# Performance work log

Measured on AMD Instinct MI355X. Metric: run time of the kernel, lower is better.

Reference implementation:

```python
import jax, jax.numpy as jnp
import numpy as np

N = 100000      # nodes
E = 1600000     # edges
D_IN = 32
D_OUT = 32
K = 2           # propagation hops; module has k+1 alpha scalars


def setup_inputs() -> dict:
    key = jax.random.key(0)
    k1, k2, k3, k4, k5 = jax.random.split(key, 5)
    feat = jax.random.normal(k1, (N, D_IN), dtype=jnp.float32)
    src = jax.random.randint(k2, (E,), 0, N, dtype=jnp.int32)
    dst = jax.random.randint(k3, (E,), 0, N, dtype=jnp.int32)
    stdv = 1.0 / np.sqrt(D_OUT)
    W = jax.random.uniform(k4, (D_OUT, D_IN), dtype=jnp.float32, minval=-stdv, maxval=stdv)
    b = jnp.zeros((D_OUT,), dtype=jnp.float32)
    stdvk = 1.0 / np.sqrt(K)
    alpha = jax.random.uniform(k5, (K + 1,), dtype=jnp.float32, minval=-stdvk, maxval=stdvk)
    return {"feat": feat, "src": src, "dst": dst, "W": W, "b": b, "alpha": alpha}


def reference(feat, src, dst, W, b, alpha):
    n = feat.shape[0]
    # in-degrees (edges point src -> dst; copy_u/sum aggregates at dst)
    deg = jax.ops.segment_sum(jnp.ones_like(dst, dtype=jnp.float32), dst, num_segments=n)
    norm = jnp.maximum(deg, 1.0)[:, None] ** -0.5  # [n,1]

    feats = [feat]
    h = feat
    for _ in range(K):
        h = h * norm                                       # pre-normalize
        h = jax.ops.segment_sum(h[src], dst, num_segments=n)  # SpMM: gather+scatter-add
        h = h * norm                                       # post-normalize
        feats.append(h)

    # result = sum_i fc(alpha_i * feat_i); bias added once per hop term (as in torch)
    result = jnp.zeros((n, W.shape[0]), dtype=jnp.float32)
    for i, f in enumerate(feats):
        result = result + (alpha[i] * f) @ W.T + b
    return result
```

## Files before the change

kernel.cpp:

```cpp
#include <hip/hip_runtime.h>

#define D 32
#define CHUNK 4096
#define BWID 512
#define BSH 9
#define SCAN_T 256
#define SCAN_V 4
#define SCAN_CHUNK 1024

__device__ __forceinline__ unsigned f2bf2(float lo, float hi) {
    union { float f; unsigned u; } a, b;
    a.f = lo; b.f = hi;
    unsigned ra = a.u + 0x7FFFu + ((a.u >> 16) & 1u);
    unsigned rb = b.u + 0x7FFFu + ((b.u >> 16) & 1u);
    return (ra >> 16) | (rb & 0xFFFF0000u);
}
__device__ __forceinline__ void bf2_unpack(unsigned u, float& lo, float& hi) {
    union { unsigned u; float f; } a, b;
    a.u = u << 16; b.u = u & 0xFFFF0000u;
    lo = a.f; hi = b.f;
}


__global__ void p1_count_kernel(const int* __restrict__ dst, int* __restrict__ cnt,
                                int E, int NB) {
    __shared__ int h[256];
    int blk = blockIdx.x, t = threadIdx.x;
    for (int i = t; i < 256; i += 256) h[i] = 0;
    __syncthreads();
    int base = blk * CHUNK;
    int end = min(base + CHUNK, E);
    int tbase = base + t * 16;
    #pragma unroll
    for (int k = 0; k < 4; ++k) {
        int a = tbase + k * 4;
        if (a + 3 < end) {
            int4 d = *(const int4*)(dst + a);
            atomicAdd(&h[d.x >> BSH], 1);
            atomicAdd(&h[d.y >> BSH], 1);
            atomicAdd(&h[d.z >> BSH], 1);
            atomicAdd(&h[d.w >> BSH], 1);
        } else {
            for (int e = a; e < end && e < a + 4; ++e) atomicAdd(&h[dst[e] >> BSH], 1);
        }
    }
    __syncthreads();
    for (int i = t; i < NB; i += 256) cnt[blk * NB + i] = h[i];
}

__global__ void red_kernel(const int* __restrict__ cnt, int* __restrict__ btot,
                           int GB, int NB) {
    __shared__ int s[256];
    int b = blockIdx.x, t = threadIdx.x;
    int acc = 0;
    for (int g = t; g < GB; g += 256) acc += cnt[g * NB + b];
    s[t] = acc;
    __syncthreads();
    for (int off = 128; off > 0; off >>= 1) {
        if (t < off) s[t] += s[t + off];
        __syncthreads();
    }
    if (t == 0) btot[b] = s[0];
}

__global__ void scanb_kernel(const int* __restrict__ btot, int* __restrict__ bbase, int NB) {
    __shared__ int s[256];
    int t = threadIdx.x;
    int v = (t < NB) ? btot[t] : 0;
    s[t] = v;
    __syncthreads();
    for (int off = 1; off < 256; off <<= 1) {
        int x = (t >= off) ? s[t - off] : 0;
        __syncthreads();
        s[t] += x;
        __syncthreads();
    }
    if (t < NB) bbase[t] = s[t] - v;
    if (t == NB - 1) bbase[NB] = s[t];
}

__global__ void off_kernel(const int* __restrict__ cnt, const int* __restrict__ bbase,
                           int* __restrict__ off, int GB, int NB) {
    __shared__ int st[256];
    int b = blockIdx.x, t = threadIdx.x;
    int g0 = 2 * t, g1 = 2 * t + 1;
    int c0 = (g0 < GB) ? cnt[g0 * NB + b] : 0;
    int c1 = (g1 < GB) ? cnt[g1 * NB + b] : 0;
    int pair = c0 + c1;
    st[t] = pair;
    __syncthreads();
    for (int o = 1; o < 256; o <<= 1) {
        int x = (t >= o) ? st[t - o] : 0;
        __syncthreads();
        st[t] += x;
        __syncthreads();
    }
    int ex = bbase[b] + st[t] - pair;
    if (g0 < GB) off[g0 * NB + b] = ex;
    if (g1 < GB) off[g1 * NB + b] = ex + c0;
}

__global__ void p3_scatter_kernel(const int* __restrict__ src, const int* __restrict__ dst,
                                  const int* __restrict__ off, unsigned* __restrict__ ebuf,
                                  int E, int NB) {
    __shared__ int cur[256];
    int blk = blockIdx.x, t = threadIdx.x;
    for (int i = t; i < NB; i += 256) cur[i] = off[blk * NB + i];
    __syncthreads();
    int base = blk * CHUNK;
    int end = min(base + CHUNK, E);
    int tbase = base + t * 16;
    #pragma unroll
    for (int k = 0; k < 4; ++k) {
        int a = tbase + k * 4;
        if (a + 3 < end) {
            int4 d = *(const int4*)(dst + a);
            int4 s = *(const int4*)(src + a);
            int p0 = atomicAdd(&cur[d.x >> BSH], 1);
            int p1 = atomicAdd(&cur[d.y >> BSH], 1);
            int p2 = atomicAdd(&cur[d.z >> BSH], 1);
            int p3 = atomicAdd(&cur[d.w >> BSH], 1);
            ebuf[p0] = ((unsigned)(d.x & (BWID - 1)) << 23) | (unsigned)s.x;
            ebuf[p1] = ((unsigned)(d.y & (BWID - 1)) << 23) | (unsigned)s.y;
            ebuf[p2] = ((unsigned)(d.z & (BWID - 1)) << 23) | (unsigned)s.z;
            ebuf[p3] = ((unsigned)(d.w & (BWID - 1)) << 23) | (unsigned)s.w;
        } else {
            for (int e = a; e < end && e < a + 4; ++e) {
                int dv = dst[e];
                int p = atomicAdd(&cur[dv >> BSH], 1);
                ebuf[p] = ((unsigned)(dv & (BWID - 1)) << 23) | (unsigned)src[e];
            }
        }
    }
}

__global__ void p4_kernel(const unsigned* __restrict__ ebuf, const int* __restrict__ bbase,
                          int* __restrict__ row_start, int* __restrict__ row_end,
                          float* __restrict__ norm, int* __restrict__ csr_src,
                          const float4* __restrict__ feat4, uint4* __restrict__ A1q, int N) {
    __shared__ int deg2[BWID];
    __shared__ int rs[BWID];
    __shared__ int st[256];
    int b = blockIdx.x, t = threadIdx.x;
    int node0 = b << BSH;
    int nn = min(BWID, N - node0);
    int e0 = bbase[b], e1 = bbase[b + 1];
    deg2[t] = 0; deg2[t + 256] = 0;
    __syncthreads();
    for (int j = e0 + t; j < e1; j += 256)
        atomicAdd(&deg2[ebuf[j] >> 23], 1);
    __syncthreads();
    int d0 = deg2[2 * t], d1 = deg2[2 * t + 1];
    int pair = d0 + d1;
    st[t] = pair;
    __syncthreads();
    for (int off = 1; off < 256; off <<= 1) {
        int v = (t >= off) ? st[t - off] : 0;
        __syncthreads();
        st[t] += v;
        __syncthreads();
    }
    int ex = st[t] - pair;
    rs[2 * t] = ex;
    rs[2 * t + 1] = ex + d0;
    __syncthreads();
    #pragma unroll
    for (int k = 0; k < 2; ++k) {
        int i = t + k * 256;
        if (i < nn) {
            int dg = deg2[i];
            int r = e0 + rs[i];
            row_start[node0 + i] = r;
            row_end[node0 + i]   = r + dg;
            norm[node0 + i] = rsqrtf(fmaxf((float)dg, 1.0f));
        }
    }
    __syncthreads();
    for (int j = e0 + t; j < e1; j += 256) {
        unsigned v = ebuf[j];
        int dl = v >> 23;
        int p = atomicAdd(&rs[dl], 1);
        csr_src[e0 + p] = (int)(v & 0x7FFFFF);
    }
    for (int c = t; c < nn * 4; c += 256) {
        int nl = c >> 2, q = c & 3;
        float nv = rsqrtf(fmaxf((float)deg2[nl], 1.0f));
        size_t rf = (size_t)(node0 + nl) * 8 + q * 2;
        float4 f0 = feat4[rf], f1 = feat4[rf + 1];
        uint4 o;
        o.x = f2bf2(f0.x * nv, f0.y * nv);
        o.y = f2bf2(f0.z * nv, f0.w * nv);
        o.z = f2bf2(f1.x * nv, f1.y * nv);
        o.w = f2bf2(f1.z * nv, f1.w * nv);
        A1q[(size_t)(node0 + nl) * 4 + q] = o;
    }
}

__global__ void degpos_kernel(const int* __restrict__ dst, int* __restrict__ deg,
                              int* __restrict__ pos, int E) {
    int t = blockIdx.x * blockDim.x + threadIdx.x;
    int base = t * 4;
    if (base + 3 < E) {
        int4 d = *(const int4*)(dst + base);
        int4 p;
        p.x = atomicAdd(&deg[d.x], 1);
        p.y = atomicAdd(&deg[d.y], 1);
        p.z = atomicAdd(&deg[d.z], 1);
        p.w = atomicAdd(&deg[d.w], 1);
        *(int4*)(pos + base) = p;
    } else if (base < E) {
        for (int e = base; e < E; ++e) pos[e] = atomicAdd(&deg[dst[e]], 1);
    }
}

__global__ void scan1_kernel(const int* __restrict__ deg, int* __restrict__ partial, int n) {
    __shared__ int sdata[SCAN_T];
    int base = blockIdx.x * SCAN_CHUNK + threadIdx.x * SCAN_V;
    int s = 0;
    #pragma unroll
    for (int k = 0; k < SCAN_V; ++k) { int i = base + k; if (i < n) s += deg[i]; }
    sdata[threadIdx.x] = s;
    __syncthreads();
    for (int off = SCAN_T / 2; off > 0; off >>= 1) {
        if (threadIdx.x < off) sdata[threadIdx.x] += sdata[threadIdx.x + off];
        __syncthreads();
    }
    if (threadIdx.x == 0) partial[blockIdx.x] = sdata[0];
}

__global__ void scan2_kernel(int* __restrict__ partial, int nb) {
    __shared__ int sdata[256];
    int v = (threadIdx.x < nb) ? partial[threadIdx.x] : 0;
    sdata[threadIdx.x] = v;
    __syncthreads();
    for (int off = 1; off < 256; off <<= 1) {
        int t = (threadIdx.x >= off) ? sdata[threadIdx.x - off] : 0;
        __syncthreads();
        sdata[threadIdx.x] += t;
        __syncthreads();
    }
    if (threadIdx.x < nb) partial[threadIdx.x] = sdata[threadIdx.x] - v;
}

__global__ void scan3_kernel(const int* __restrict__ deg, const int* __restrict__ partial,
                             int* __restrict__ row_start, int* __restrict__ row_end,
                             float* __restrict__ norm, int n) {
    __shared__ int sdata[SCAN_T];
    int base = blockIdx.x * SCAN_CHUNK + threadIdx.x * SCAN_V;
    int v[SCAN_V];
    int s = 0;
    #pragma unroll
    for (int k = 0; k < SCAN_V; ++k) { int i = base + k; v[k] = (i < n) ? deg[i] : 0; s += v[k]; }
    int self = s;
    sdata[threadIdx.x] = s;
    __syncthreads();
    for (int off = 1; off < SCAN_T; off <<= 1) {
        int t = (threadIdx.x >= off) ? sdata[threadIdx.x - off] : 0;
        __syncthreads();
        sdata[threadIdx.x] += t;
        __syncthreads();
    }
    int run = partial[blockIdx.x] + sdata[threadIdx.x] - self;
    #pragma unroll
    for (int k = 0; k < SCAN_V; ++k) {
        int i = base + k;
        if (i < n) {
            row_start[i] = run;
            row_end[i]   = run + v[k];
            norm[i] = rsqrtf(fmaxf((float)v[k], 1.0f));
            run += v[k];
        }
    }
}

__global__ void fillA_kernel(const int* __restrict__ src, const int* __restrict__ dst,
                             const int* __restrict__ pos, const int* __restrict__ row_start,
                             int* __restrict__ csr_src, int E) {
    int t = blockIdx.x * blockDim.x + threadIdx.x;
    int base = t * 4;
    if (base + 3 < E) {
        int4 d = *(const int4*)(dst + base);
        int4 p = *(const int4*)(pos + base);
        int4 s = *(const int4*)(src + base);
        csr_src[row_start[d.x] + p.x] = s.x;
        csr_src[row_start[d.y] + p.y] = s.y;
        csr_src[row_start[d.z] + p.z] = s.z;
        csr_src[row_start[d.w] + p.w] = s.w;
    } else if (base < E) {
        for (int e = base; e < E; ++e)
            csr_src[row_start[dst[e]] + pos[e]] = src[e];
    }
}

__global__ void prep_kernel(const float4* __restrict__ feat4, const float* __restrict__ norm,
                            uint4* __restrict__ A1q, int nchunk) {
    int i = blockIdx.x * blockDim.x + threadIdx.x;
    if (i >= nchunk) return;
    int v = i >> 2;
    float nv = norm[v];
    float4 f0 = feat4[(size_t)i * 2], f1 = feat4[(size_t)i * 2 + 1];
    uint4 o;
    o.x = f2bf2(f0.x * nv, f0.y * nv);
    o.y = f2bf2(f0.z * nv, f0.w * nv);
    o.z = f2bf2(f1.x * nv, f1.y * nv);
    o.w = f2bf2(f1.z * nv, f1.w * nv);
    A1q[i] = o;
}


#define ACC_EDGE(V)                                              \
    { float lo_, hi_;                                            \
      bf2_unpack((V).x, lo_, hi_); acc[0] += lo_; acc[1] += hi_; \
      bf2_unpack((V).y, lo_, hi_); acc[2] += lo_; acc[3] += hi_; \
      bf2_unpack((V).z, lo_, hi_); acc[4] += lo_; acc[5] += hi_; \
      bf2_unpack((V).w, lo_, hi_); acc[6] += lo_; acc[7] += hi_; }

__global__ __launch_bounds__(256) void gather1_kernel(
        const int* __restrict__ row_start, const int* __restrict__ row_end,
        const int* __restrict__ csr_src, const uint4* __restrict__ A1q,
        const float4* __restrict__ feat4, const float* __restrict__ norm,
        const float* __restrict__ alpha, float4* __restrict__ G,
        uint4* __restrict__ A2q, int n) {
    int wave = blockIdx.x * (blockDim.x >> 6) + (threadIdx.x >> 6);
    int lane = threadIdx.x & 63;
    int g  = lane >> 4;
    int eo = (lane >> 2) & 3;
    int q  = lane & 3;
    int r = wave * 4 + g;
    int s0 = 0, e1 = 0;
    if (r < n) { s0 = row_start[r]; e1 = row_end[r]; }
    float acc[8];
    #pragma unroll
    for (int i = 0; i < 8; ++i) acc[i] = 0.f;
    int j = s0 + eo;
    for (; j + 4 < e1; j += 8) {
        int sa = csr_src[j];
        int sb = csr_src[j + 4];
        uint4 va = A1q[(size_t)sa * 4 + q];
        uint4 vb = A1q[(size_t)sb * 4 + q];
        ACC_EDGE(va);
        ACC_EDGE(vb);
    }
    if (j < e1) {
        int sa = csr_src[j];
        uint4 va = A1q[(size_t)sa * 4 + q];
        ACC_EDGE(va);
    }
    #pragma unroll
    for (int i = 0; i < 8; ++i) {
        acc[i] += __shfl_xor(acc[i], 4);
        acc[i] += __shfl_xor(acc[i], 8);
    }
    if (eo == 0 && r < n) {
        float nv = norm[r];
        float a0 = alpha[0], a1 = alpha[1];
        size_t rf = (size_t)r * 8 + q * 2;
        float4 f0 = feat4[rf], f1 = feat4[rf + 1];
        float h[8];
        #pragma unroll
        for (int i = 0; i < 8; ++i) h[i] = acc[i] * nv;
        G[rf]     = make_float4(fmaf(a1, h[0], a0 * f0.x), fmaf(a1, h[1], a0 * f0.y),
                                fmaf(a1, h[2], a0 * f0.z), fmaf(a1, h[3], a0 * f0.w));
        G[rf + 1] = make_float4(fmaf(a1, h[4], a0 * f1.x), fmaf(a1, h[5], a0 * f1.y),
                                fmaf(a1, h[6], a0 * f1.z), fmaf(a1, h[7], a0 * f1.w));
        uint4 o;
        o.x = f2bf2(h[0] * nv, h[1] * nv);
        o.y = f2bf2(h[2] * nv, h[3] * nv);
        o.z = f2bf2(h[4] * nv, h[5] * nv);
        o.w = f2bf2(h[6] * nv, h[7] * nv);
        A2q[(size_t)r * 4 + q] = o;
    }
}

__global__ __launch_bounds__(256) void gather2_kernel(
        const int* __restrict__ row_start, const int* __restrict__ row_end,
        const int* __restrict__ csr_src, const uint4* __restrict__ A2q,
        const float* __restrict__ norm, const float* __restrict__ alpha,
        const float* __restrict__ W, const float* __restrict__ b,
        float4* __restrict__ G, int n) {
    __shared__ float Wl[D][D + 1];
    __shared__ float pbuf[4][4][D];
    int tid = threadIdx.x;
    for (int k = tid; k < D * D; k += 256) Wl[k >> 5][k & 31] = W[k];
    __syncthreads();

    int wv = tid >> 6;
    int wave = blockIdx.x * 4 + wv;
    int lane = tid & 63;
    int g  = lane >> 4;
    int eo = (lane >> 2) & 3;
    int q  = lane & 3;
    int r = wave * 4 + g;
    int s0 = 0, e1 = 0;
    if (r < n) { s0 = row_start[r]; e1 = row_end[r]; }
    float acc[8];
    #pragma unroll
    for (int i = 0; i < 8; ++i) acc[i] = 0.f;
    int j = s0 + eo;
    for (; j + 4 < e1; j += 8) {
        int sa = csr_src[j];
        int sb = csr_src[j + 4];
        uint4 va = A2q[(size_t)sa * 4 + q];
        uint4 vb = A2q[(size_t)sb * 4 + q];
        ACC_EDGE(va);
        ACC_EDGE(vb);
    }
    if (j < e1) {
        int sa = csr_src[j];
        uint4 va = A2q[(size_t)sa * 4 + q];
        ACC_EDGE(va);
    }
    #pragma unroll
    for (int i = 0; i < 8; ++i) {
        acc[i] += __shfl_xor(acc[i], 4);
        acc[i] += __shfl_xor(acc[i], 8);
    }
    if (eo == 0 && r < n) {
        float nv = norm[r];
        float a2 = alpha[2];
        size_t rf = (size_t)r * 8 + q * 2;
        float4 g0 = G[rf], g1 = G[rf + 1];
        float4 p0 = make_float4(fmaf(a2, acc[0] * nv, g0.x), fmaf(a2, acc[1] * nv, g0.y),
                                fmaf(a2, acc[2] * nv, g0.z), fmaf(a2, acc[3] * nv, g0.w));
        float4 p1 = make_float4(fmaf(a2, acc[4] * nv, g1.x), fmaf(a2, acc[5] * nv, g1.y),
                                fmaf(a2, acc[6] * nv, g1.z), fmaf(a2, acc[7] * nv, g1.w));
        *(float4*)&pbuf[wv][g][q * 8]     = p0;
        *(float4*)&pbuf[wv][g][q * 8 + 4] = p1;
    }
    asm volatile("s_waitcnt lgkmcnt(0)" ::: "memory");

    int o  = lane & 31;
    int rr = lane >> 5;
    #pragma unroll
    for (int rp = 0; rp < 2; ++rp) {
        int gg = rp * 2 + rr;
        int row = wave * 4 + gg;
        if (row < n) {
            float acco = 0.f;
            #pragma unroll
            for (int k = 0; k < D; ++k)
                acco = fmaf(pbuf[wv][gg][k], Wl[o][k], acco);
            ((float*)G)[(size_t)row * D + o] = acco + 3.0f * b[o];
        }
    }
}

extern "C" void kernel_launch(void* const* d_in, const int* in_sizes, int n_in,
                              void* d_out, int out_size, void* d_ws, size_t ws_size,
                              hipStream_t stream) {
    const float* feat  = (const float*)d_in[0];
    const int*   src   = (const int*)  d_in[1];
    const int*   dst   = (const int*)  d_in[2];
    const float* W     = (const float*)d_in[3];
    const float* b     = (const float*)d_in[4];
    const float* alpha = (const float*)d_in[5];

    const int N  = in_sizes[0] / D;
    const int E  = in_sizes[1];
    const int BT = 256;
    const int NB = (N + BWID - 1) >> BSH;
    const int GB = (E + CHUNK - 1) / CHUNK;
    const int gblocks = (N + 15) / 16;
    float4* G = (float4*)d_out;

    size_t needA = ((size_t)32 * N + 2 * (size_t)GB * NB + 2 * NB + 1
                    + 2 * (size_t)E + 3 * (size_t)N) * 4;

    if (ws_size >= needA && NB <= 256 && GB <= 512 && N < (1 << 23)) {
        unsigned* A1q       = (unsigned*)d_ws;
        unsigned* A2q       = A1q + (size_t)16 * N;
        int*      cnt       = (int*)(A2q + (size_t)16 * N);
        int*      off       = cnt + (size_t)GB * NB;
        int*      btot      = off + (size_t)GB * NB;
        int*      bbase     = btot + NB;
        unsigned* ebuf      = (unsigned*)(bbase + NB + 1);
        int*      csr_src   = (int*)(ebuf + E);
        int*      row_start = csr_src + E;
        int*      row_end   = row_start + N;
        float*    norm      = (float*)(row_end + N);

        p1_count_kernel<<<GB, BT, 0, stream>>>(dst, cnt, E, NB);
        red_kernel<<<NB, BT, 0, stream>>>(cnt, btot, GB, NB);
        scanb_kernel<<<1, BT, 0, stream>>>(btot, bbase, NB);
        off_kernel<<<NB, BT, 0, stream>>>(cnt, bbase, off, GB, NB);
        p3_scatter_kernel<<<GB, BT, 0, stream>>>(src, dst, off, ebuf, E, NB);
        p4_kernel<<<NB, BT, 0, stream>>>(ebuf, bbase, row_start, row_end, norm, csr_src,
                                         (const float4*)feat, (uint4*)A1q, N);
        gather1_kernel<<<gblocks, BT, 0, stream>>>(row_start, row_end, csr_src,
                                                   (const uint4*)A1q, (const float4*)feat,
                                                   norm, alpha, G, (uint4*)A2q, N);
        gather2_kernel<<<gblocks, BT, 0, stream>>>(row_start, row_end, csr_src,
                                                   (const uint4*)A2q, norm, alpha,
                                                   W, b, G, N);
    } else {
        const int nb = (N + SCAN_CHUNK - 1) / SCAN_CHUNK;
        const int e4blocks = ((E + 3) / 4 + BT - 1) / BT;
        unsigned* A1q       = (unsigned*)d_ws;
        unsigned* A2q       = A1q + (size_t)16 * N;
        int*      deg       = (int*)(A2q + (size_t)16 * N);
        int*      pos       = deg + N;
        int*      partial   = pos + E;
        int*      row_start = partial + 256;
        int*      row_end   = row_start + N;
        int*      csr_src   = row_end + N;
        float*    norm      = (float*)(csr_src + E);

        hipMemsetAsync(deg, 0, (size_t)N * sizeof(int), stream);
        degpos_kernel<<<e4blocks, BT, 0, stream>>>(dst, deg, pos, E);
        scan1_kernel<<<nb, SCAN_T, 0, stream>>>(deg, partial, N);
        scan2_kernel<<<1, 256, 0, stream>>>(partial, nb);
        scan3_kernel<<<nb, SCAN_T, 0, stream>>>(deg, partial, row_start, row_end, norm, N);
        fillA_kernel<<<e4blocks, BT, 0, stream>>>(src, dst, pos, row_start, csr_src, E);
        prep_kernel<<<(4 * N + BT - 1) / BT, BT, 0, stream>>>(
            (const float4*)feat, norm, (uint4*)A1q, 4 * N);
        gather1_kernel<<<gblocks, BT, 0, stream>>>(row_start, row_end, csr_src,
                                                   (const uint4*)A1q, (const float4*)feat,
                                                   norm, alpha, G, (uint4*)A2q, N);
        gather2_kernel<<<gblocks, BT, 0, stream>>>(row_start, row_end, csr_src,
                                                   (const uint4*)A2q, norm, alpha,
                                                   W, b, G, N);
    }
}
```

Measured before the change: 113.3 us.

## Split feature gathers into two 16-column halves with separate GEMM pass

The bf16 propagated features are stored as two half-width arrays of 16 columns each. Each gather hop runs twice, once per half, so the random-access working set per pass is halved and should fit better in L2/MALL. Each lane now covers 8 edges and 2 quads, and the fused W projection moves out of gather2 into a standalone GEMM kernel. This costs extra launches, reading the CSR index arrays twice per hop, and an extra read/write pass over the output.

```diff
diff --git a/kernel.cpp b/kernel.cpp
--- a/kernel.cpp
+++ b/kernel.cpp
@@ -137,7 +137,8 @@
 __global__ void p4_kernel(const unsigned* __restrict__ ebuf, const int* __restrict__ bbase,
                           int* __restrict__ row_start, int* __restrict__ row_end,
                           float* __restrict__ norm, int* __restrict__ csr_src,
-                          const float4* __restrict__ feat4, uint4* __restrict__ A1q, int N) {
+                          const float* __restrict__ feat,
+                          unsigned* __restrict__ A1h0, unsigned* __restrict__ A1h1, int N) {
     __shared__ int deg2[BWID];
     __shared__ int rs[BWID];
     __shared__ int st[256];
@@ -182,17 +183,14 @@
         int p = atomicAdd(&rs[dl], 1);
         csr_src[e0 + p] = (int)(v & 0x7FFFFF);
     }
-    for (int c = t; c < nn * 4; c += 256) {
-        int nl = c >> 2, q = c & 3;
-        float nv = rsqrtf(fmaxf((float)deg2[nl], 1.0f));
-        size_t rf = (size_t)(node0 + nl) * 8 + q * 2;
-        float4 f0 = feat4[rf], f1 = feat4[rf + 1];
-        uint4 o;
-        o.x = f2bf2(f0.x * nv, f0.y * nv);
-        o.y = f2bf2(f0.z * nv, f0.w * nv);
-        o.z = f2bf2(f1.x * nv, f1.y * nv);
-        o.w = f2bf2(f1.z * nv, f1.w * nv);
-        A1q[(size_t)(node0 + nl) * 4 + q] = o;
+    for (int c = t; c < nn * 16; c += 256) {
+        int i = c >> 4, k = c & 15;
+        float nv = rsqrtf(fmaxf((float)deg2[i], 1.0f));
+        size_t fi = (size_t)(node0 + i) * D + 2 * k;
+        float2 f = *(const float2*)(feat + fi);
+        unsigned u = f2bf2(f.x * nv, f.y * nv);
+        if (k < 8) A1h0[(size_t)(node0 + i) * 8 + k] = u;
+        else       A1h1[(size_t)(node0 + i) * 8 + (k - 8)] = u;
     }
 }
 
@@ -292,23 +290,22 @@
     }
 }
 
-__global__ void prep_kernel(const float4* __restrict__ feat4, const float* __restrict__ norm,
-                            uint4* __restrict__ A1q, int nchunk) {
-    int i = blockIdx.x * blockDim.x + threadIdx.x;
-    if (i >= nchunk) return;
-    int v = i >> 2;
+__global__ void prep_kernel(const float* __restrict__ feat, const float* __restrict__ norm,
+                            unsigned* __restrict__ A1h0, unsigned* __restrict__ A1h1,
+                            int total) {
+    int c = blockIdx.x * blockDim.x + threadIdx.x;
+    if (c >= total) return;
+    int v = c >> 4, k = c & 15;
     float nv = norm[v];
-    float4 f0 = feat4[(size_t)i * 2], f1 = feat4[(size_t)i * 2 + 1];
-    uint4 o;
-    o.x = f2bf2(f0.x * nv, f0.y * nv);
-    o.y = f2bf2(f0.z * nv, f0.w * nv);
-    o.z = f2bf2(f1.x * nv, f1.y * nv);
-    o.w = f2bf2(f1.z * nv, f1.w * nv);
-    A1q[i] = o;
-}
-
-
-#define ACC_EDGE(V)                                              \
+    size_t fi = (size_t)v * D + 2 * k;
+    float2 f = *(const float2*)(feat + fi);
+    unsigned u = f2bf2(f.x * nv, f.y * nv);
+    if (k < 8) A1h0[(size_t)v * 8 + k] = u;
+    else       A1h1[(size_t)v * 8 + (k - 8)] = u;
+}
+
+
+#define ACC_H(V)                                                 \
     { float lo_, hi_;                                            \
       bf2_unpack((V).x, lo_, hi_); acc[0] += lo_; acc[1] += hi_; \
       bf2_unpack((V).y, lo_, hi_); acc[2] += lo_; acc[3] += hi_; \
@@ -317,15 +314,15 @@
 
 __global__ __launch_bounds__(256) void gather1_kernel(
         const int* __restrict__ row_start, const int* __restrict__ row_end,
-        const int* __restrict__ csr_src, const uint4* __restrict__ A1q,
+        const int* __restrict__ csr_src, const uint4* __restrict__ Ah,
         const float4* __restrict__ feat4, const float* __restrict__ norm,
         const float* __restrict__ alpha, float4* __restrict__ G,
-        uint4* __restrict__ A2q, int n) {
+        uint4* __restrict__ A2h, int n, int h) {
     int wave = blockIdx.x * (blockDim.x >> 6) + (threadIdx.x >> 6);
     int lane = threadIdx.x & 63;
     int g  = lane >> 4;
-    int eo = (lane >> 2) & 3;
-    int q  = lane & 3;
+    int eo = (lane >> 1) & 7;
+    int q  = lane & 1;
     int r = wave * 4 + g;
     int s0 = 0, e1 = 0;
     if (r < n) { s0 = row_start[r]; e1 = row_end[r]; }
@@ -333,63 +330,56 @@
     #pragma unroll
     for (int i = 0; i < 8; ++i) acc[i] = 0.f;
     int j = s0 + eo;
-    for (; j + 4 < e1; j += 8) {
+    for (; j + 8 < e1; j += 16) {
         int sa = csr_src[j];
-        int sb = csr_src[j + 4];
-        uint4 va = A1q[(size_t)sa * 4 + q];
-        uint4 vb = A1q[(size_t)sb * 4 + q];
-        ACC_EDGE(va);
-        ACC_EDGE(vb);
+        int sb = csr_src[j + 8];
+        uint4 va = Ah[(size_t)sa * 2 + q];
+        uint4 vb = Ah[(size_t)sb * 2 + q];
+        ACC_H(va);
+        ACC_H(vb);
     }
     if (j < e1) {
         int sa = csr_src[j];
-        uint4 va = A1q[(size_t)sa * 4 + q];
-        ACC_EDGE(va);
+        uint4 va = Ah[(size_t)sa * 2 + q];
+        ACC_H(va);
     }
     #pragma unroll
     for (int i = 0; i < 8; ++i) {
+        acc[i] += __shfl_xor(acc[i], 2);
         acc[i] += __shfl_xor(acc[i], 4);
         acc[i] += __shfl_xor(acc[i], 8);
     }
     if (eo == 0 && r < n) {
         float nv = norm[r];
         float a0 = alpha[0], a1 = alpha[1];
-        size_t rf = (size_t)r * 8 + q * 2;
-        float4 f0 = feat4[rf], f1 = feat4[rf + 1];
-        float h[8];
+        size_t base = (size_t)r * 8 + h * 4 + q * 2;
+        float4 f0 = feat4[base], f1 = feat4[base + 1];
+        float hh[8];
         #pragma unroll
-        for (int i = 0; i < 8; ++i) h[i] = acc[i] * nv;
-        G[rf]     = make_float4(fmaf(a1, h[0], a0 * f0.x), fmaf(a1, h[1], a0 * f0.y),
-                                fmaf(a1, h[2], a0 * f0.z), fmaf(a1, h[3], a0 * f0.w));
-        G[rf + 1] = make_float4(fmaf(a1, h[4], a0 * f1.x), fmaf(a1, h[5], a0 * f1.y),
-                                fmaf(a1, h[6], a0 * f1.z), fmaf(a1, h[7], a0 * f1.w));
+        for (int i = 0; i < 8; ++i) hh[i] = acc[i] * nv;
+        G[base]     = make_float4(fmaf(a1, hh[0], a0 * f0.x), fmaf(a1, hh[1], a0 * f0.y),
+                                  fmaf(a1, hh[2], a0 * f0.z), fmaf(a1, hh[3], a0 * f0.w));
+        G[base + 1] = make_float4(fmaf(a1, hh[4], a0 * f1.x), fmaf(a1, hh[5], a0 * f1.y),
+                                  fmaf(a1, hh[6], a0 * f1.z), fmaf(a1, hh[7], a0 * f1.w));
         uint4 o;
-        o.x = f2bf2(h[0] * nv, h[1] * nv);
-        o.y = f2bf2(h[2] * nv, h[3] * nv);
-        o.z = f2bf2(h[4] * nv, h[5] * nv);
-        o.w = f2bf2(h[6] * nv, h[7] * nv);
-        A2q[(size_t)r * 4 + q] = o;
+        o.x = f2bf2(hh[0] * nv, hh[1] * nv);
+        o.y = f2bf2(hh[2] * nv, hh[3] * nv);
+        o.z = f2bf2(hh[4] * nv, hh[5] * nv);
+        o.w = f2bf2(hh[6] * nv, hh[7] * nv);
+        A2h[(size_t)r * 2 + q] = o;
     }
 }
 
 __global__ __launch_bounds__(256) void gather2_kernel(
         const int* __restrict__ row_start, const int* __restrict__ row_end,
-        const int* __restrict__ csr_src, const uint4* __restrict__ A2q,
+        const int* __restrict__ csr_src, const uint4* __restrict__ Ah,
         const float* __restrict__ norm, const float* __restrict__ alpha,
-        const float* __restrict__ W, const float* __restrict__ b,
-        float4* __restrict__ G, int n) {
-    __shared__ float Wl[D][D + 1];
-    __shared__ float pbuf[4][4][D];
-    int tid = threadIdx.x;
-    for (int k = tid; k < D * D; k += 256) Wl[k >> 5][k & 31] = W[k];
-    __syncthreads();
-
-    int wv = tid >> 6;
-    int wave = blockIdx.x * 4 + wv;
-    int lane = tid & 63;
+        float4* __restrict__ G, int n, int h) {
+    int wave = blockIdx.x * (blockDim.x >> 6) + (threadIdx.x >> 6);
+    int lane = threadIdx.x & 63;
     int g  = lane >> 4;
-    int eo = (lane >> 2) & 3;
-    int q  = lane & 3;
+    int eo = (lane >> 1) & 7;
+    int q  = lane & 1;
     int r = wave * 4 + g;
     int s0 = 0, e1 = 0;
     if (r < n) { s0 = row_start[r]; e1 = row_end[r]; }
@@ -397,51 +387,55 @@
     #pragma unroll
     for (int i = 0; i < 8; ++i) acc[i] = 0.f;
     int j = s0 + eo;
-    for (; j + 4 < e1; j += 8) {
+    for (; j + 8 < e1; j += 16) {
         int sa = csr_src[j];
-        int sb = csr_src[j + 4];
-        uint4 va = A2q[(size_t)sa * 4 + q];
-        uint4 vb = A2q[(size_t)sb * 4 + q];
-        ACC_EDGE(va);
-        ACC_EDGE(vb);
+        int sb = csr_src[j + 8];
+        uint4 va = Ah[(size_t)sa * 2 + q];
+        uint4 vb = Ah[(size_t)sb * 2 + q];
+        ACC_H(va);
+        ACC_H(vb);
     }
     if (j < e1) {
         int sa = csr_src[j];
-        uint4 va = A2q[(size_t)sa * 4 + q];
-        ACC_EDGE(va);
+        uint4 va = Ah[(size_t)sa * 2 + q];
+        ACC_H(va);
     }
     #pragma unroll
     for (int i = 0; i < 8; ++i) {
+        acc[i] += __shfl_xor(acc[i], 2);
         acc[i] += __shfl_xor(acc[i], 4);
         acc[i] += __shfl_xor(acc[i], 8);
     }
     if (eo == 0 && r < n) {
         float nv = norm[r];
         float a2 = alpha[2];
-        size_t rf = (size_t)r * 8 + q * 2;
-        float4 g0 = G[rf], g1 = G[rf + 1];
-        float4 p0 = make_float4(fmaf(a2, acc[0] * nv, g0.x), fmaf(a2, acc[1] * nv, g0.y),
-                                fmaf(a2, acc[2] * nv, g0.z), fmaf(a2, acc[3] * nv, g0.w));
-        float4 p1 = make_float4(fmaf(a2, acc[4] * nv, g1.x), fmaf(a2, acc[5] * nv, g1.y),
-                                fmaf(a2, acc[6] * nv, g1.z), fmaf(a2, acc[7] * nv, g1.w));
-        *(float4*)&pbuf[wv][g][q * 8]     = p0;
-        *(float4*)&pbuf[wv][g][q * 8 + 4] = p1;
-    }
-    asm volatile("s_waitcnt lgkmcnt(0)" ::: "memory");
-
-    int o  = lane & 31;
-    int rr = lane >> 5;
-    #pragma unroll
-    for (int rp = 0; rp < 2; ++rp) {
-        int gg = rp * 2 + rr;
-        int row = wave * 4 + gg;
-        if (row < n) {
-            float acco = 0.f;
-            #pragma unroll
-            for (int k = 0; k < D; ++k)
-                acco = fmaf(pbuf[wv][gg][k], Wl[o][k], acco);
-            ((float*)G)[(size_t)row * D + o] = acco + 3.0f * b[o];
-        }
+        size_t base = (size_t)r * 8 + h * 4 + q * 2;
+        float4 g0 = G[base], g1 = G[base + 1];
+        G[base]     = make_float4(fmaf(a2, acc[0] * nv, g0.x), fmaf(a2, acc[1] * nv, g0.y),
+                                  fmaf(a2, acc[2] * nv, g0.z), fmaf(a2, acc[3] * nv, g0.w));
+        G[base + 1] = make_float4(fmaf(a2, acc[4] * nv, g1.x), fmaf(a2, acc[5] * nv, g1.y),
+                                  fmaf(a2, acc[6] * nv, g1.z), fmaf(a2, acc[7] * nv, g1.w));
+    }
+}
+
+__global__ void gemm_kernel(float* __restrict__ g,
+                            const float* __restrict__ W,
+                            const float* __restrict__ b, int n) {
+    __shared__ float Wl[D][D + 1];
+    __shared__ float gl[8][D];
+    int tid = threadIdx.x;
+    for (int k = tid; k < D * D; k += 256) Wl[k >> 5][k & 31] = W[k];
+    int v0 = blockIdx.x * 8;
+    int lr = tid >> 5;
+    int o  = tid & 31;
+    int v = v0 + lr;
+    if (v < n) gl[lr][o] = g[(size_t)v * D + o];
+    __syncthreads();
+    if (v < n) {
+        float acc = 3.0f * b[o];
+        #pragma unroll
+        for (int k = 0; k < D; ++k) acc = fmaf(gl[lr][k], Wl[o][k], acc);
+        g[(size_t)v * D + o] = acc;
     }
 }
 
@@ -461,15 +455,18 @@
     const int NB = (N + BWID - 1) >> BSH;
     const int GB = (E + CHUNK - 1) / CHUNK;
     const int gblocks = (N + 15) / 16;
+    const int gemm_blocks = (N + 7) / 8;
     float4* G = (float4*)d_out;
 
     size_t needA = ((size_t)32 * N + 2 * (size_t)GB * NB + 2 * NB + 1
                     + 2 * (size_t)E + 3 * (size_t)N) * 4;
 
     if (ws_size >= needA && NB <= 256 && GB <= 512 && N < (1 << 23)) {
-        unsigned* A1q       = (unsigned*)d_ws;
-        unsigned* A2q       = A1q + (size_t)16 * N;
-        int*      cnt       = (int*)(A2q + (size_t)16 * N);
+        unsigned* A1h0      = (unsigned*)d_ws;
+        unsigned* A1h1      = A1h0 + (size_t)8 * N;
+        unsigned* A2h0      = A1h1 + (size_t)8 * N;
+        unsigned* A2h1      = A2h0 + (size_t)8 * N;
+        int*      cnt       = (int*)(A2h1 + (size_t)8 * N);
         int*      off       = cnt + (size_t)GB * NB;
         int*      btot      = off + (size_t)GB * NB;
         int*      bbase     = btot + NB;
@@ -485,19 +482,27 @@
         off_kernel<<<NB, BT, 0, stream>>>(cnt, bbase, off, GB, NB);
         p3_scatter_kernel<<<GB, BT, 0, stream>>>(src, dst, off, ebuf, E, NB);
         p4_kernel<<<NB, BT, 0, stream>>>(ebuf, bbase, row_start, row_end, norm, csr_src,
-                                         (const float4*)feat, (uint4*)A1q, N);
+                                         feat, A1h0, A1h1, N);
+
         gather1_kernel<<<gblocks, BT, 0, stream>>>(row_start, row_end, csr_src,
-                                                   (const uint4*)A1q, (const float4*)feat,
-                                                   norm, alpha, G, (uint4*)A2q, N);
+                                                   (const uint4*)A1h0, (const float4*)feat,
+                                                   norm, alpha, G, (uint4*)A2h0, N, 0);
+        gather1_kernel<<<gblocks, BT, 0, stream>>>(row_start, row_end, csr_src,
+                                                   (const uint4*)A1h1, (const float4*)feat,
+                                                   norm, alpha, G, (uint4*)A2h1, N, 1);
         gather2_kernel<<<gblocks, BT, 0, stream>>>(row_start, row_end, csr_src,
-                                                   (const uint4*)A2q, norm, alpha,
-                                                   W, b, G, N);
+                                                   (const uint4*)A2h0, norm, alpha, G, N, 0);
+        gather2_kernel<<<gblocks, BT, 0, stream>>>(row_start, row_end, csr_src,
+                                                   (const uint4*)A2h1, norm, alpha, G, N, 1);
+        gemm_kernel<<<gemm_blocks, BT, 0, stream>>>((float*)G, W, b, N);
     } else {
         const int nb = (N + SCAN_CHUNK - 1) / SCAN_CHUNK;
         const int e4blocks = ((E + 3) / 4 + BT - 1) / BT;
-        unsigned* A1q       = (unsigned*)d_ws;
-        unsigned* A2q       = A1q + (size_t)16 * N;
-        int*      deg       = (int*)(A2q + (size_t)16 * N);
+        unsigned* A1h0      = (unsigned*)d_ws;
+        unsigned* A1h1      = A1h0 + (size_t)8 * N;
+        unsigned* A2h0      = A1h1 + (size_t)8 * N;
+        unsigned* A2h1      = A2h0 + (size_t)8 * N;
+        int*      deg       = (int*)(A2h1 + (size_t)8 * N);
         int*      pos       = deg + N;
         int*      partial   = pos + E;
         int*      row_start = partial + 256;
@@ -511,13 +516,18 @@
         scan2_kernel<<<1, 256, 0, stream>>>(partial, nb);
         scan3_kernel<<<nb, SCAN_T, 0, stream>>>(deg, partial, row_start, row_end, norm, N);
         fillA_kernel<<<e4blocks, BT, 0, stream>>>(src, dst, pos, row_start, csr_src, E);
-        prep_kernel<<<(4 * N + BT - 1) / BT, BT, 0, stream>>>(
-            (const float4*)feat, norm, (uint4*)A1q, 4 * N);
+        prep_kernel<<<(16 * N + BT - 1) / BT, BT, 0, stream>>>(feat, norm, A1h0, A1h1, 16 * N);
+
         gather1_kernel<<<gblocks, BT, 0, stream>>>(row_start, row_end, csr_src,
-                                                   (const uint4*)A1q, (const float4*)feat,
-                                                   norm, alpha, G, (uint4*)A2q, N);
+                                                   (const uint4*)A1h0, (const float4*)feat,
+                                                   norm, alpha, G, (uint4*)A2h0, N, 0);
+        gather1_kernel<<<gblocks, BT, 0, stream>>>(row_start, row_end, csr_src,
+                                                   (const uint4*)A1h1, (const float4*)feat,
+                                                   norm, alpha, G, (uint4*)A2h1, N, 1);
         gather2_kernel<<<gblocks, BT, 0, stream>>>(row_start, row_end, csr_src,
-                                                   (const uint4*)A2q, norm, alpha,
-                                                   W, b, G, N);
-    }
-}
+                                                   (const uint4*)A2h0, norm, alpha, G, N, 0);
+        gather2_kernel<<<gblocks, BT, 0, stream>>>(row_start, row_end, csr_src,
+                                                   (const uint4*)A2h1, norm, alpha, G, N, 1);
+        gemm_kernel<<<gemm_blocks, BT, 0, stream>>>((float*)G, W, b, N);
+    }
+}
```

Result: slower. 150.7 us (+33.0%).
